# Kernel tuning notes

Measured on AMD Instinct MI355X. Metric: run time of the kernel, lower is better.

## Reference

```python
import jax, jax.numpy as jnp
import numpy as np

N = 100_000      # nodes
E = 1_600_000    # edges (before self-loops)
F_IN = 128       # num_features
H = 128          # nhid
G = 512          # graphs in batch
C = 10           # num_classes
EPS = 1e-5       # BatchNorm eps


def setup_inputs() -> dict:
    key = jax.random.key(0)
    ks = jax.random.split(key, 24)
    x = jax.random.normal(ks[0], (N, F_IN), jnp.float32)
    edge_index = jax.random.randint(ks[1], (2, E), 0, N, dtype=jnp.int64)
    batch = jnp.sort(jax.random.randint(ks[2], (N,), 0, G, dtype=jnp.int64))

    def lin(k, fi, fo):
        return jax.random.normal(k, (fi, fo), jnp.float32) / np.sqrt(fi).astype(np.float32)

    inp = dict(x=x, edge_index=edge_index, batch=batch)
    inp.update(
        W1=lin(ks[3], F_IN, H), b1=jnp.zeros((H,), jnp.float32),
        g1=jnp.ones((H,), jnp.float32), be1=jnp.zeros((H,), jnp.float32),
        W2=lin(ks[4], H, H), b2=jnp.zeros((H,), jnp.float32),
        g2=jnp.ones((H,), jnp.float32), be2=jnp.zeros((H,), jnp.float32),
        W3=lin(ks[5], H, H), b3=jnp.zeros((H,), jnp.float32),
        g3=jnp.ones((H,), jnp.float32), be3=jnp.zeros((H,), jnp.float32),
        gp=jnp.ones((H,), jnp.float32), bep=jnp.zeros((H,), jnp.float32),
        lw1=lin(ks[6], H, H), lb1=jnp.zeros((H,), jnp.float32),
        lw2=lin(ks[7], H, C), lb2=jnp.zeros((C,), jnp.float32),
    )
    return inp


def _batchnorm(h, g, b):
    # training-mode BatchNorm1d: batch stats, biased variance
    m = h.mean(axis=0)
    v = h.var(axis=0)
    return g * (h - m) * jax.lax.rsqrt(v + EPS) + b


def _gcn(h, W, b, src, dst, norm, n):
    # GCNConv: h @ W, then normalized gather-scatter aggregation
    h = h @ W
    msg = h[src] * norm[:, None]                     # [E+N, H] gather
    out = jax.ops.segment_sum(msg, dst, num_segments=n)
    return out + b


def reference(x, edge_index, batch, W1, b1, g1, be1, W2, b2, g2, be2,
              W3, b3, g3, be3, gp, bep, lw1, lb1, lw2, lb2):
    n = x.shape[0]
    loops = jnp.arange(n, dtype=edge_index.dtype)
    src = jnp.concatenate([edge_index[0], loops])
    dst = jnp.concatenate([edge_index[1], loops])
    # symmetric normalization D^{-1/2} (A+I) D^{-1/2}
    deg = jax.ops.segment_sum(jnp.ones_like(src, dtype=x.dtype), dst, num_segments=n)
    dis = jnp.where(deg > 0, jax.lax.rsqrt(jnp.maximum(deg, 1.0)), 0.0)
    norm = dis[src] * dis[dst]

    h = jax.nn.relu(_batchnorm(_gcn(x, W1, b1, src, dst, norm, n), g1, be1))
    h = jax.nn.relu(_batchnorm(_gcn(h, W2, b2, src, dst, norm, n), g2, be2))
    h = jax.nn.relu(_batchnorm(_gcn(h, W3, b3, src, dst, norm, n), g3, be3))

    # global_mean_pool over graph ids
    counts = jax.ops.segment_sum(jnp.ones((n,), x.dtype), batch, num_segments=G)
    pooled = jax.ops.segment_sum(h, batch, num_segments=G) / jnp.maximum(counts, 1.0)[:, None]

    z = _batchnorm(pooled, gp, bep)
    z = jax.nn.relu(z @ lw1 + lb1)
    # dropout_ratio=0.0 -> identity
    z = z @ lw2 + lb2
    return jax.nn.log_softmax(z, axis=-1)
```

## Files before the change

kernel.cpp:

```cpp
#include <hip/hip_runtime.h>
#include <hip/hip_bf16.h>
#include <cstdint>

#define HDIM 128

typedef __bf16 bf16x8 __attribute__((ext_vector_type(8)));
typedef unsigned short usx8 __attribute__((ext_vector_type(8)));
typedef float fx4 __attribute__((ext_vector_type(4)));

__device__ __forceinline__ float bf2f(unsigned short u) {
    unsigned int x = ((unsigned int)u) << 16;
    return __uint_as_float(x);
}
__device__ __forceinline__ unsigned short f2bf(float f) {
    unsigned int x = __float_as_uint(f);
    x += 0x7fffu + ((x >> 16) & 1u);
    return (unsigned short)(x >> 16);
}

__device__ __forceinline__ void detect_local(const unsigned int* xw, const unsigned int* eiw,
                                             int& f0, int& f1) {
    int sane = 0;
    for (int k = 0; k < 64; k++) {
        unsigned int w = xw[k];
        unsigned short ss[2] = {(unsigned short)(w & 0xffffu), (unsigned short)(w >> 16)};
        for (int q = 0; q < 2; q++) {
            int e = (ss[q] >> 7) & 0xFF;
            if ((ss[q] & 0x7fffu) == 0 || (e >= 100 && e <= 140)) sane++;
        }
    }
    f0 = (sane >= 110) ? 1 : 0;
    int zeros = 0;
    for (int k = 1; k < 64; k += 2)
        if (eiw[k] == 0) zeros++;
    f1 = (zeros >= 24) ? 1 : 0;
}

struct ParamTab {
    const void* p[15];
    int n[15];
    int off[15];
};

__global__ void phase1(const unsigned int* __restrict__ xw, const unsigned int* __restrict__ eiw,
                       const void* __restrict__ ei, const void* __restrict__ batch,
                       const void* __restrict__ W1, const void* __restrict__ W2,
                       const void* __restrict__ W3, ParamTab tab, int* __restrict__ flags,
                       float* __restrict__ gsumAll, int* __restrict__ Ct,
                       unsigned short* __restrict__ wconv, unsigned short* __restrict__ Wf,
                       int* __restrict__ goff, int* __restrict__ gcnt, int E, int N, int G,
                       int NB, int ntiles, int TILE) {
    __shared__ int h[1024];
    __shared__ int lf0s, lf1s;
    int b = blockIdx.x, t = threadIdx.x;
    if (t == 0) {
        int a0, a1;
        detect_local(xw, eiw, a0, a1);
        lf0s = a0;
        lf1s = a1;
    }
    __syncthreads();
    int lf0 = lf0s, lf1 = lf1s;
    if (b < ntiles) {
        for (int i = t; i < NB; i += 256) h[i] = 0;
        __syncthreads();
        int base = b * TILE;
        for (int i = t; i < TILE; i += 256) {
            int idx = base + i;
            if (idx < E) {
                int d = lf1 ? (int)((const long long*)ei)[(size_t)E + idx]
                            : ((const int*)ei)[(size_t)E + idx];
                atomicAdd(&h[d >> 9], 1);
            }
        }
        __syncthreads();
        for (int k = t; k < NB; k += 256) Ct[k * ntiles + b] = h[k];
    } else if (b < ntiles + 15) {
        int pb = b - ntiles;
        const void* src = tab.p[pb];
        int n = tab.n[pb];
        unsigned short* o = wconv + tab.off[pb];
        if (lf0) {
            const unsigned short* s = (const unsigned short*)src;
            for (int i = t; i < n; i += 256) o[i] = s[i];
        } else {
            const float* s = (const float*)src;
            for (int i = t; i < n; i += 256) o[i] = f2bf(s[i]);
        }
    } else if (b < ntiles + 17) {
        int gi = (b - ntiles - 15) * 256 + t;
        if (gi < G) {
            auto getb = [&](int i) -> int {
                return lf1 ? (int)((const long long*)batch)[i] : ((const int*)batch)[i];
            };
            auto lower = [&](int val) -> int {
                int lo = 0, hi = N;
                while (lo < hi) {
                    int mid = (lo + hi) >> 1;
                    if (getb(mid) < val) lo = mid + 1;
                    else hi = mid;
                }
                return lo;
            };
            int lo = lower(gi), hi = lower(gi + 1);
            goff[gi] = lo;
            gcnt[gi] = hi - lo;
        }
    } else if (b < ntiles + 17 + 24) {
        int idx = (b - ntiles - 17) * 256 + t;
        int layer = idx >> 11;
        int rem = idx & 2047;
        int kt = rem >> 9;
        int nt = (rem >> 6) & 7;
        int lane = rem & 63;
        const void* W = (layer == 0) ? W1 : ((layer == 1) ? W2 : W3);
        int row = lane & 15, quad = lane >> 4;
        unsigned short* o = Wf + ((size_t)layer * 2048 + (size_t)((kt * 8 + nt) * 64 + lane)) * 8;
#pragma unroll
        for (int j = 0; j < 8; j++) {
            int k = kt * 32 + quad * 8 + j;
            int off = k * HDIM + nt * 16 + row;
            o[j] = lf0 ? ((const unsigned short*)W)[off] : f2bf(((const float*)W)[off]);
        }
    } else {
        for (int i = t; i < 768; i += 256) gsumAll[i] = 0.f;
        if (t == 0) {
            flags[0] = lf0;
            flags[1] = lf1;
        }
    }
}

__global__ void scanA(const int* __restrict__ d, int* __restrict__ part, int L) {
    __shared__ int ls[256];
    int b = blockIdx.x, t = threadIdx.x;
    int base = b * 2048;
    int s = 0;
    for (int j = t; j < 2048; j += 256) {
        int i = base + j;
        if (i < L) s += d[i];
    }
    ls[t] = s;
    __syncthreads();
    for (int o = 128; o > 0; o >>= 1) {
        if (t < o) ls[t] += ls[t + o];
        __syncthreads();
    }
    if (t == 0) part[b] = ls[0];
}
__global__ void scan2(int* part, int nb) {
    __shared__ int ls[128];
    int t = threadIdx.x;
    int orig = (t < nb) ? part[t] : 0;
    ls[t] = orig;
    __syncthreads();
    for (int o = 1; o < 128; o <<= 1) {
        int v = (t >= o) ? ls[t - o] : 0;
        __syncthreads();
        ls[t] += v;
        __syncthreads();
    }
    if (t < nb) part[t] = ls[t] - orig;
}
__global__ void scanC(int* __restrict__ d, const int* __restrict__ part, int L) {
    __shared__ int ls[256];
    __shared__ int excl[256];
    int b = blockIdx.x, t = threadIdx.x;
    int i0 = b * 2048 + t * 8;
    int v[8];
    int s = 0;
#pragma unroll
    for (int q = 0; q < 8; q++) {
        v[q] = (i0 + q < L) ? d[i0 + q] : 0;
        s += v[q];
    }
    ls[t] = s;
    __syncthreads();
    if (t == 0) {
        int a = 0;
        for (int j = 0; j < 256; j++) { excl[j] = a; a += ls[j]; }
    }
    __syncthreads();
    int base = part[b] + excl[t];
#pragma unroll
    for (int q = 0; q < 8; q++) {
        if (i0 + q < L) d[i0 + q] = base;
        base += v[q];
    }
}

__global__ void p1_scatter(const void* __restrict__ ei, const int* __restrict__ flags,
                           const int* __restrict__ Ct, unsigned int* __restrict__ pairs, int E,
                           int NB, int ntiles, int TILE) {
    __shared__ int cur[1024];
    int tile = blockIdx.x, t = threadIdx.x;
    for (int i = t; i < NB; i += 256) cur[i] = Ct[i * ntiles + tile];
    __syncthreads();
    int base = tile * TILE;
    bool i64 = flags[1] != 0;
    for (int i = t; i < TILE; i += 256) {
        int idx = base + i;
        if (idx < E) {
            int s, d;
            if (i64) {
                s = (int)((const long long*)ei)[idx];
                d = (int)((const long long*)ei)[(size_t)E + idx];
            } else {
                s = ((const int*)ei)[idx];
                d = ((const int*)ei)[(size_t)E + idx];
            }
            int pos = atomicAdd(&cur[d >> 9], 1);
            pairs[pos] = ((unsigned)(d & 511) << 23) | (unsigned)s;
        }
    }
}

__global__ void p2_build(const unsigned int* __restrict__ pairs, const int* __restrict__ Ct,
                         int* __restrict__ csrc, int* __restrict__ offs, int* __restrict__ cnt,
                         float* __restrict__ dis, int E, int N, int NB, int ntiles) {
    __shared__ int hist[512];
    __shared__ int start[512];
    __shared__ int cur[512];
    __shared__ int ps[256];
    int b = blockIdx.x, t = threadIdx.x;
    int node0 = b * 512;
    for (int i = t; i < 512; i += 256) hist[i] = 0;
    __syncthreads();
    int lo = Ct[b * ntiles];
    int hi = (b + 1 < NB) ? Ct[(b + 1) * ntiles] : E;
    for (int i = lo + t; i < hi; i += 256) {
        atomicAdd(&hist[pairs[i] >> 23], 1);
    }
    __syncthreads();
    ps[t] = hist[2 * t] + hist[2 * t + 1];
    __syncthreads();
    for (int o = 1; o < 256; o <<= 1) {
        int v = (t >= o) ? ps[t - o] : 0;
        __syncthreads();
        ps[t] += v;
        __syncthreads();
    }
    int e = t ? ps[t - 1] : 0;
    start[2 * t] = e;
    start[2 * t + 1] = e + hist[2 * t];
    __syncthreads();
    for (int i = t; i < 512; i += 256) {
        cur[i] = 0;
        int node = node0 + i;
        if (node < N) {
            offs[node] = lo + start[i];
            cnt[node] = hist[i];
            dis[node] = rsqrtf((float)(hist[i] + 1));
        }
    }
    __syncthreads();
    for (int i = lo + t; i < hi; i += 256) {
        unsigned int p = pairs[i];
        int l = p >> 23;
        int pos = lo + start[l] + atomicAdd(&cur[l], 1);
        csrc[pos] = (int)(p & 0x7fffffu);
    }
}

__global__ __launch_bounds__(256) void mm_mfma(const void* __restrict__ A,
                                               const unsigned short* __restrict__ Wf,
                                               unsigned short* __restrict__ C, int M,
                                               const float* __restrict__ sc,
                                               const float* __restrict__ sh,
                                               const float* __restrict__ dis,
                                               const int* __restrict__ flags, int l0mode) {
    int gid = blockIdx.x * blockDim.x + threadIdx.x;
    int wave = gid >> 6;
    int lane = threadIdx.x & 63;
    int m0 = wave * 16;
    if (m0 >= M) return;
    int row = lane & 15, quad = lane >> 4;
    bool xfp32 = l0mode && !flags[0];
    const unsigned short* arow =
        (const unsigned short*)A + (size_t)(m0 + row) * HDIM + quad * 8;
    const float* arowf = (const float*)A + (size_t)(m0 + row) * HDIM + quad * 8;
    fx4 acc[8];
#pragma unroll
    for (int t = 0; t < 8; t++) acc[t] = (fx4){0.f, 0.f, 0.f, 0.f};
#pragma unroll
    for (int kt = 0; kt < 4; kt++) {
        bf16x8 a;
        if (xfp32) {
            fx4 f0 = *(const fx4*)(arowf + kt * 32);
            fx4 f1 = *(const fx4*)(arowf + kt * 32 + 4);
            usx8 t;
#pragma unroll
            for (int q = 0; q < 4; q++) t[q] = f2bf(f0[q]);
#pragma unroll
            for (int q = 0; q < 4; q++) t[4 + q] = f2bf(f1[q]);
            a = __builtin_bit_cast(bf16x8, t);
        } else {
            usx8 raw = *(const usx8*)(arow + kt * 32);
            if (!l0mode) {
                int col = kt * 32 + quad * 8;
                fx4 s0 = *(const fx4*)(sc + col);
                fx4 s1 = *(const fx4*)(sc + col + 4);
                fx4 h0 = *(const fx4*)(sh + col);
                fx4 h1 = *(const fx4*)(sh + col + 4);
                usx8 t;
#pragma unroll
                for (int q = 0; q < 4; q++)
                    t[q] = f2bf(fmaxf(s0[q] * bf2f(raw[q]) + h0[q], 0.f));
#pragma unroll
                for (int q = 0; q < 4; q++)
                    t[4 + q] = f2bf(fmaxf(s1[q] * bf2f(raw[4 + q]) + h1[q], 0.f));
                a = __builtin_bit_cast(bf16x8, t);
            } else {
                a = __builtin_bit_cast(bf16x8, raw);
            }
        }
        const unsigned short* wf = Wf + ((size_t)(kt * 8) * 64 + lane) * 8;
#pragma unroll
        for (int nt = 0; nt < 8; nt++) {
            bf16x8 b = __builtin_bit_cast(bf16x8, *(const usx8*)(wf + (size_t)nt * 64 * 8));
            acc[nt] = __builtin_amdgcn_mfma_f32_16x16x32_bf16(a, b, acc[nt], 0, 0, 0);
        }
    }
    float dsc[4];
#pragma unroll
    for (int r = 0; r < 4; r++) dsc[r] = dis[m0 + quad * 4 + r];
#pragma unroll
    for (int nt = 0; nt < 8; nt++) {
        int col = nt * 16 + row;
#pragma unroll
        for (int r = 0; r < 4; r++) {
            int m = m0 + quad * 4 + r;
            C[(size_t)m * HDIM + col] = f2bf(acc[nt][r] * dsc[r]);
        }
    }
}

__global__ __launch_bounds__(256) void aggregate(const unsigned short* __restrict__ hw,
                                                 const float* __restrict__ dis,
                                                 const int* __restrict__ offs,
                                                 const int* __restrict__ cnt,
                                                 const int* __restrict__ csrc,
                                                 const unsigned short* __restrict__ bias,
                                                 unsigned short* __restrict__ agg, int n) {
    int wv = (blockIdx.x * blockDim.x + threadIdx.x) >> 6;
    int lane = threadIdx.x & 63;
    int grp = lane >> 4, sub = lane & 15;
    int node = wv * 4 + grp;
    if (node >= n) return;
    int colb = sub * 8;
    usx8 sv = *(const usx8*)(hw + (size_t)node * HDIM + colb);
    float a[8];
#pragma unroll
    for (int q = 0; q < 8; q++) a[q] = bf2f(sv[q]);
    int o = offs[node], c = cnt[node];
    int s0 = (c > 0) ? csrc[o] : 0;
    int s1 = (c > 1) ? csrc[o + 1] : 0;
    int j = 0;
    while (j < c) {
        usx8 v0 = *(const usx8*)(hw + (size_t)s0 * HDIM + colb);
        usx8 v1 = *(const usx8*)(hw + (size_t)s1 * HDIM + colb);
        int s2 = (j + 2 < c) ? csrc[o + j + 2] : 0;
        int s3 = (j + 3 < c) ? csrc[o + j + 3] : 0;
#pragma unroll
        for (int q = 0; q < 8; q++) a[q] += bf2f(v0[q]);
        if (j + 1 < c) {
#pragma unroll
            for (int q = 0; q < 8; q++) a[q] += bf2f(v1[q]);
        }
        s0 = s2;
        s1 = s3;
        j += 2;
    }
    float di = dis[node];
    usx8 bv = *(const usx8*)(bias + colb);
    usx8 ov;
#pragma unroll
    for (int q = 0; q < 8; q++) ov[q] = f2bf(bf2f(bv[q]) + di * a[q]);
    *(usx8*)(agg + (size_t)node * HDIM + colb) = ov;
}

__global__ void col_stats(const unsigned short* __restrict__ agg, float* __restrict__ gsum,
                          float* __restrict__ gsq, int n) {
    int t = threadIdx.x;
    int c = t & 127, p = t >> 7;
    float s = 0.f, s2 = 0.f;
    int stride = gridDim.x * 2;
    for (int r = blockIdx.x * 2 + p; r < n; r += stride) {
        float v = bf2f(agg[(size_t)r * HDIM + c]);
        s += v;
        s2 += v * v;
    }
    __shared__ float ls[256], ls2[256];
    ls[t] = s;
    ls2[t] = s2;
    __syncthreads();
    if (t < 128) {
        atomicAdd(&gsum[t], ls[t] + ls[t + 128]);
        atomicAdd(&gsq[t], ls2[t] + ls2[t + 128]);
    }
}
__global__ void bn_finalize(const float* __restrict__ gsum, const float* __restrict__ gsq,
                            const unsigned short* __restrict__ g,
                            const unsigned short* __restrict__ be,
                            float* __restrict__ sc, float* __restrict__ sh, float invn) {
    int c = threadIdx.x;
    if (c < 128) {
        float m = gsum[c] * invn;
        float v = gsq[c] * invn - m * m;
        float s = bf2f(g[c]) * rsqrtf(v + 1e-5f);
        sc[c] = s;
        sh[c] = bf2f(be[c]) - m * s;
    }
}

__global__ void pool(const unsigned short* __restrict__ hin, const int* __restrict__ goff,
                     const int* __restrict__ gcnt, const float* __restrict__ sc,
                     const float* __restrict__ sh, float* __restrict__ pooled) {
    int g = blockIdx.x, t = threadIdx.x;
    int c = t & 127, p = t >> 7;
    float scale = sc[c], shift = sh[c];
    int s = goff[g], cn = gcnt[g];
    float acc = 0.f;
    for (int r = s + p; r < s + cn; r += 2)
        acc += fmaxf(scale * bf2f(hin[(size_t)r * HDIM + c]) + shift, 0.f);
    __shared__ float ls[256];
    ls[t] = acc;
    __syncthreads();
    if (t < 128) pooled[(size_t)g * HDIM + t] = (ls[t] + ls[t + 128]) / fmaxf((float)cn, 1.f);
}
__global__ void pooled_bn(const float* __restrict__ pooled, const unsigned short* __restrict__ g,
                          const unsigned short* __restrict__ be, float* __restrict__ psc,
                          float* __restrict__ psh, int G_) {
    int t = threadIdx.x;
    int c = t & 127, p = t >> 7;
    float s = 0.f, s2 = 0.f;
    for (int r = p; r < G_; r += 4) {
        float v = pooled[(size_t)r * HDIM + c];
        s += v;
        s2 += v * v;
    }
    __shared__ float ls[512], ls2[512];
    ls[t] = s;
    ls2[t] = s2;
    __syncthreads();
    if (t < 128) {
        float S = ls[t] + ls[t + 128] + ls[t + 256] + ls[t + 384];
        float S2 = ls2[t] + ls2[t + 128] + ls2[t + 256] + ls2[t + 384];
        float m = S / (float)G_;
        float v = S2 / (float)G_ - m * m;
        float sc = bf2f(g[t]) * rsqrtf(v + 1e-5f);
        psc[t] = sc;
        psh[t] = bf2f(be[t]) - m * sc;
    }
}
__global__ void mlp1(const float* __restrict__ pooled, const float* __restrict__ psc,
                     const float* __restrict__ psh, const unsigned short* __restrict__ lw1,
                     const unsigned short* __restrict__ lb1, float* __restrict__ z1) {
    int r = blockIdx.x, t = threadIdx.x;
    __shared__ float row[128];
    row[t] = psc[t] * pooled[(size_t)r * HDIM + t] + psh[t];
    __syncthreads();
    float acc = bf2f(lb1[t]);
    for (int k = 0; k < 128; k++) acc += row[k] * bf2f(lw1[k * HDIM + t]);
    z1[(size_t)r * HDIM + t] = fmaxf(acc, 0.f);
}
__global__ void mlp2(const float* __restrict__ z1, const unsigned short* __restrict__ lw2,
                     const unsigned short* __restrict__ lb2, void* __restrict__ out,
                     const int* __restrict__ flags) {
    int r = blockIdx.x, t = threadIdx.x;
    __shared__ float row[128];
    __shared__ float z2[10];
    __shared__ float lse;
    row[t] = z1[(size_t)r * HDIM + t];
    __syncthreads();
    if (t < 10) {
        float a = bf2f(lb2[t]);
        for (int k = 0; k < 128; k++) a += row[k] * bf2f(lw2[k * 10 + t]);
        z2[t] = a;
    }
    __syncthreads();
    if (t == 0) {
        float m = z2[0];
        for (int j = 1; j < 10; j++) m = fmaxf(m, z2[j]);
        float s = 0.f;
        for (int j = 0; j < 10; j++) s += expf(z2[j] - m);
        lse = m + logf(s);
    }
    __syncthreads();
    if (t < 10) {
        float v = z2[t] - lse;
        if (flags[0]) ((unsigned short*)out)[r * 10 + t] = f2bf(v);
        else ((float*)out)[r * 10 + t] = v;
    }
}

extern "C" void kernel_launch(void* const* d_in, const int* in_sizes, int n_in,
                              void* d_out, int out_size, void* d_ws, size_t ws_size,
                              hipStream_t stream) {
    const void* x = d_in[0];
    const void* ei = d_in[1];
    const void* batch = d_in[2];

    int N_ = in_sizes[2];
    int E_ = in_sizes[1] / 2;
    int G_ = out_size / 10;

    const int TILE = 4096;
    int NB = (N_ + 511) / 512;
    int ntiles = (E_ + TILE - 1) / TILE;
    int L = NB * ntiles;
    int nscan = (L + 2047) / 2048;

    char* ws = (char*)d_ws;
    auto alloc = [&](size_t bytes) -> char* {
        char* p = ws;
        ws += (bytes + 255) & ~(size_t)255;
        return p;
    };
    int* flags = (int*)alloc(256);
    float* dis = (float*)alloc((size_t)N_ * 4);
    int* offs = (int*)alloc((size_t)N_ * 4);
    int* cnt = (int*)alloc((size_t)N_ * 4);
    int* part = (int*)alloc(4096);
    int* Ct = (int*)alloc((size_t)L * 4);
    unsigned int* pairs = (unsigned int*)alloc((size_t)E_ * 4);
    int* csrc = (int*)alloc((size_t)E_ * 4);
    unsigned short* hw = (unsigned short*)alloc((size_t)N_ * HDIM * 2);
    unsigned short* aggbuf = (unsigned short*)alloc((size_t)N_ * HDIM * 2);
    unsigned short* wconv = (unsigned short*)alloc(70000 * 2);
    unsigned short* wfrag = (unsigned short*)alloc(3 * HDIM * HDIM * 2);
    float* gsumAll = (float*)alloc(768 * 4);
    float* bsc = (float*)alloc(128 * 4);
    float* bsh = (float*)alloc(128 * 4);
    int* gcnt = (int*)alloc((size_t)G_ * 4);
    int* goff = (int*)alloc((size_t)G_ * 4);
    float* pooled = (float*)alloc((size_t)G_ * HDIM * 4);
    float* psc = (float*)alloc(128 * 4);
    float* psh = (float*)alloc(128 * 4);
    float* z1 = (float*)alloc((size_t)G_ * HDIM * 4);

    const int oB = 49152;
    const int oLB1 = oB + 1408;
    const int oLW1 = oLB1 + 128;
    const int oLW2 = oLW1 + 16384;
    const int oLB2 = oLW2 + 1280;

    ParamTab tab;
    const int srcIdx[15] = {4, 5, 6, 8, 9, 10, 12, 13, 14, 15, 16, 18, 17, 19, 20};
    const int dstOff[15] = {oB + 0, oB + 128, oB + 256,
                            oB + 384, oB + 512, oB + 640,
                            oB + 768, oB + 896, oB + 1024,
                            oB + 1152, oB + 1280,
                            oLB1, oLW1, oLW2, oLB2};
    for (int i = 0; i < 15; i++) {
        tab.p[i] = d_in[srcIdx[i]];
        tab.n[i] = in_sizes[srcIdx[i]];
        tab.off[i] = dstOff[i];
    }

    int gb = (G_ + 255) / 256;
    int p1_grid = ntiles + 15 + 2 + 24 + 1;
    phase1<<<p1_grid, 256, 0, stream>>>((const unsigned int*)x, (const unsigned int*)ei, ei,
                                        batch, d_in[3], d_in[7], d_in[11], tab, flags, gsumAll,
                                        Ct, wconv, wfrag, goff, gcnt, E_, N_, G_, NB, ntiles,
                                        TILE);
    (void)gb;

    scanA<<<nscan, 256, 0, stream>>>(Ct, part, L);
    scan2<<<1, 128, 0, stream>>>(part, nscan);
    scanC<<<nscan, 256, 0, stream>>>(Ct, part, L);
    p1_scatter<<<ntiles, 256, 0, stream>>>(ei, flags, Ct, pairs, E_, NB, ntiles, TILE);
    p2_build<<<NB, 256, 0, stream>>>(pairs, Ct, csrc, offs, cnt, dis, E_, N_, NB, ntiles);

    int mm_blocks = (((N_ + 15) / 16) * 64 + 255) / 256;
    int agg_blocks = (N_ + 15) / 16;
    float invn = 1.f / (float)N_;

    for (int l = 0; l < 3; l++) {
        const void* A = (l == 0) ? x : (const void*)aggbuf;
        mm_mfma<<<mm_blocks, 256, 0, stream>>>(A, wfrag + (size_t)l * HDIM * HDIM, hw, N_,
                                               bsc, bsh, dis, flags, (l == 0) ? 1 : 0);
        aggregate<<<agg_blocks, 256, 0, stream>>>(hw, dis, offs, cnt, csrc,
                                                  wconv + oB + l * 384, aggbuf, N_);
        float* gsum = gsumAll + l * 256;
        col_stats<<<512, 256, 0, stream>>>(aggbuf, gsum, gsum + 128, N_);
        bn_finalize<<<1, 128, 0, stream>>>(gsum, gsum + 128, wconv + oB + l * 384 + 128,
                                           wconv + oB + l * 384 + 256, bsc, bsh, invn);
    }

    pool<<<G_, 256, 0, stream>>>(aggbuf, goff, gcnt, bsc, bsh, pooled);
    pooled_bn<<<1, 512, 0, stream>>>(pooled, wconv + oB + 1152, wconv + oB + 1280, psc, psh, G_);
    mlp1<<<G_, 128, 0, stream>>>(pooled, psc, psh, wconv + oLW1, wconv + oLB1, z1);
    mlp2<<<G_, 128, 0, stream>>>(z1, wconv + oLW2, wconv + oLB2, d_out, flags);
}
```

Measured before the change: 612.8 us.

## Fuse BN stats into aggregation, BN finalize into matmul, and simplify CSR scan

Column statistics for BatchNorm are now accumulated inside the aggregation kernel, a grid-stride loop with 768 blocks that spreads its atomics across 8 replicas. This removes the separate col_stats pass over the 100k×128 activation. BN finalize moves into the prologue of the next matmul and of the pool kernel, the two MLP kernels are merged into one, and the three-kernel scan becomes a per-bucket scan with block totals re-scanned inside consumers. The matmul also stages its output through LDS so that global stores are coalesced 16-byte writes. In exchange, every block redundantly recomputes the small scale/shift and prefix-sum values, and the aggregation gather is unrolled to four edges per step.

```diff
diff --git a/kernel.cpp b/kernel.cpp
--- a/kernel.cpp
+++ b/kernel.cpp
@@ -123,7 +123,7 @@
             o[j] = lf0 ? ((const unsigned short*)W)[off] : f2bf(((const float*)W)[off]);
         }
     } else {
-        for (int i = t; i < 768; i += 256) gsumAll[i] = 0.f;
+        for (int i = t; i < 6144; i += 256) gsumAll[i] = 0.f;
         if (t == 0) {
             flags[0] = lf0;
             flags[1] = lf1;
@@ -131,70 +131,39 @@
     }
 }
 
-__global__ void scanA(const int* __restrict__ d, int* __restrict__ part, int L) {
-    __shared__ int ls[256];
+__global__ void s1_scan(int* __restrict__ Ct, int* __restrict__ btot, int NB, int ntiles) {
+    __shared__ int buf[512];
     int b = blockIdx.x, t = threadIdx.x;
-    int base = b * 2048;
-    int s = 0;
-    for (int j = t; j < 2048; j += 256) {
-        int i = base + j;
-        if (i < L) s += d[i];
-    }
-    ls[t] = s;
-    __syncthreads();
-    for (int o = 128; o > 0; o >>= 1) {
-        if (t < o) ls[t] += ls[t + o];
-        __syncthreads();
-    }
-    if (t == 0) part[b] = ls[0];
-}
-__global__ void scan2(int* part, int nb) {
-    __shared__ int ls[128];
-    int t = threadIdx.x;
-    int orig = (t < nb) ? part[t] : 0;
-    ls[t] = orig;
-    __syncthreads();
-    for (int o = 1; o < 128; o <<= 1) {
-        int v = (t >= o) ? ls[t - o] : 0;
-        __syncthreads();
-        ls[t] += v;
-        __syncthreads();
-    }
-    if (t < nb) part[t] = ls[t] - orig;
-}
-__global__ void scanC(int* __restrict__ d, const int* __restrict__ part, int L) {
-    __shared__ int ls[256];
-    __shared__ int excl[256];
-    int b = blockIdx.x, t = threadIdx.x;
-    int i0 = b * 2048 + t * 8;
-    int v[8];
-    int s = 0;
-#pragma unroll
-    for (int q = 0; q < 8; q++) {
-        v[q] = (i0 + q < L) ? d[i0 + q] : 0;
-        s += v[q];
-    }
-    ls[t] = s;
-    __syncthreads();
-    if (t == 0) {
-        int a = 0;
-        for (int j = 0; j < 256; j++) { excl[j] = a; a += ls[j]; }
-    }
-    __syncthreads();
-    int base = part[b] + excl[t];
-#pragma unroll
-    for (int q = 0; q < 8; q++) {
-        if (i0 + q < L) d[i0 + q] = base;
-        base += v[q];
-    }
+    int v = (t < ntiles) ? Ct[b * ntiles + t] : 0;
+    buf[t] = v;
+    __syncthreads();
+    for (int o = 1; o < 512; o <<= 1) {
+        int a = (t >= o) ? buf[t - o] : 0;
+        __syncthreads();
+        buf[t] += a;
+        __syncthreads();
+    }
+    if (t < ntiles) Ct[b * ntiles + t] = buf[t] - v;
+    if (t == 0) btot[b] = buf[511];
 }
 
 __global__ void p1_scatter(const void* __restrict__ ei, const int* __restrict__ flags,
-                           const int* __restrict__ Ct, unsigned int* __restrict__ pairs, int E,
-                           int NB, int ntiles, int TILE) {
+                           const int* __restrict__ Ct, const int* __restrict__ btot,
+                           unsigned int* __restrict__ pairs, int E, int NB, int ntiles,
+                           int TILE) {
     __shared__ int cur[1024];
+    __shared__ int bb[256];
     int tile = blockIdx.x, t = threadIdx.x;
-    for (int i = t; i < NB; i += 256) cur[i] = Ct[i * ntiles + tile];
+    int v = (t < NB) ? btot[t] : 0;
+    bb[t] = v;
+    __syncthreads();
+    for (int o = 1; o < 256; o <<= 1) {
+        int a = (t >= o) ? bb[t - o] : 0;
+        __syncthreads();
+        bb[t] += a;
+        __syncthreads();
+    }
+    if (t < NB) cur[t] = (bb[t] - v) + Ct[t * ntiles + tile];
     __syncthreads();
     int base = tile * TILE;
     bool i64 = flags[1] != 0;
@@ -215,19 +184,31 @@
     }
 }
 
-__global__ void p2_build(const unsigned int* __restrict__ pairs, const int* __restrict__ Ct,
+__global__ void p2_build(const unsigned int* __restrict__ pairs, const int* __restrict__ btot,
                          int* __restrict__ csrc, int* __restrict__ offs, int* __restrict__ cnt,
-                         float* __restrict__ dis, int E, int N, int NB, int ntiles) {
+                         float* __restrict__ dis, int E, int N, int NB) {
     __shared__ int hist[512];
     __shared__ int start[512];
     __shared__ int cur[512];
     __shared__ int ps[256];
+    __shared__ int bb[256];
+    __shared__ int sh_excl[256];
     int b = blockIdx.x, t = threadIdx.x;
     int node0 = b * 512;
+    int v = (t < NB) ? btot[t] : 0;
+    bb[t] = v;
+    __syncthreads();
+    for (int o = 1; o < 256; o <<= 1) {
+        int a = (t >= o) ? bb[t - o] : 0;
+        __syncthreads();
+        bb[t] += a;
+        __syncthreads();
+    }
+    sh_excl[t] = bb[t] - v;
     for (int i = t; i < 512; i += 256) hist[i] = 0;
     __syncthreads();
-    int lo = Ct[b * ntiles];
-    int hi = (b + 1 < NB) ? Ct[(b + 1) * ntiles] : E;
+    int lo = sh_excl[b];
+    int hi = lo + ((b < NB) ? btot[b] : 0);
     for (int i = lo + t; i < hi; i += 256) {
         atomicAdd(&hist[pairs[i] >> 23], 1);
     }
@@ -235,9 +216,9 @@
     ps[t] = hist[2 * t] + hist[2 * t + 1];
     __syncthreads();
     for (int o = 1; o < 256; o <<= 1) {
-        int v = (t >= o) ? ps[t - o] : 0;
-        __syncthreads();
-        ps[t] += v;
+        int a = (t >= o) ? ps[t - o] : 0;
+        __syncthreads();
+        ps[t] += a;
         __syncthreads();
     }
     int e = t ? ps[t - 1] : 0;
@@ -265,51 +246,70 @@
 __global__ __launch_bounds__(256) void mm_mfma(const void* __restrict__ A,
                                                const unsigned short* __restrict__ Wf,
                                                unsigned short* __restrict__ C, int M,
-                                               const float* __restrict__ sc,
-                                               const float* __restrict__ sh,
+                                               const float* __restrict__ gsumPrev,
+                                               const unsigned short* __restrict__ gamma,
+                                               const unsigned short* __restrict__ beta,
                                                const float* __restrict__ dis,
-                                               const int* __restrict__ flags, int l0mode) {
-    int gid = blockIdx.x * blockDim.x + threadIdx.x;
+                                               const int* __restrict__ flags, int l0mode,
+                                               float invn) {
+    __shared__ float scs[128], shs[128];
+    __shared__ unsigned short ldsC[4 * 16 * 136];
+    int t = threadIdx.x;
+    if (!l0mode && t < 128) {
+        float s = 0.f, s2 = 0.f;
+#pragma unroll
+        for (int r = 0; r < 8; r++) {
+            s += gsumPrev[r * 256 + t];
+            s2 += gsumPrev[r * 256 + 128 + t];
+        }
+        float m = s * invn;
+        float vv = s2 * invn - m * m;
+        float sc = bf2f(gamma[t]) * rsqrtf(vv + 1e-5f);
+        scs[t] = sc;
+        shs[t] = bf2f(beta[t]) - m * sc;
+    }
+    __syncthreads();
+    int gid = blockIdx.x * blockDim.x + t;
     int wave = gid >> 6;
-    int lane = threadIdx.x & 63;
+    int lane = t & 63;
+    int wv = t >> 6;
     int m0 = wave * 16;
     if (m0 >= M) return;
     int row = lane & 15, quad = lane >> 4;
     bool xfp32 = l0mode && !flags[0];
-    const unsigned short* arow =
-        (const unsigned short*)A + (size_t)(m0 + row) * HDIM + quad * 8;
+    const unsigned short* arow = (const unsigned short*)A + (size_t)(m0 + row) * HDIM + quad * 8;
     const float* arowf = (const float*)A + (size_t)(m0 + row) * HDIM + quad * 8;
     fx4 acc[8];
 #pragma unroll
-    for (int t = 0; t < 8; t++) acc[t] = (fx4){0.f, 0.f, 0.f, 0.f};
+    for (int k = 0; k < 8; k++) acc[k] = (fx4){0.f, 0.f, 0.f, 0.f};
 #pragma unroll
     for (int kt = 0; kt < 4; kt++) {
         bf16x8 a;
         if (xfp32) {
             fx4 f0 = *(const fx4*)(arowf + kt * 32);
             fx4 f1 = *(const fx4*)(arowf + kt * 32 + 4);
-            usx8 t;
-#pragma unroll
-            for (int q = 0; q < 4; q++) t[q] = f2bf(f0[q]);
-#pragma unroll
-            for (int q = 0; q < 4; q++) t[4 + q] = f2bf(f1[q]);
-            a = __builtin_bit_cast(bf16x8, t);
+            usx8 tt;
+#pragma unroll
+            for (int q = 0; q < 4; q++) tt[q] = f2bf(f0[q]);
+#pragma unroll
+            for (int q = 0; q < 4; q++) tt[4 + q] = f2bf(f1[q]);
+            a = __builtin_bit_cast(bf16x8, tt);
         } else {
             usx8 raw = *(const usx8*)(arow + kt * 32);
             if (!l0mode) {
                 int col = kt * 32 + quad * 8;
-                fx4 s0 = *(const fx4*)(sc + col);
-                fx4 s1 = *(const fx4*)(sc + col + 4);
-                fx4 h0 = *(const fx4*)(sh + col);
-                fx4 h1 = *(const fx4*)(sh + col + 4);
-                usx8 t;
+                fx4 s0 = *(const fx4*)&scs[col];
+                fx4 s1 = *(const fx4*)&scs[col + 4];
+                fx4 h0 = *(const fx4*)&shs[col];
+                fx4 h1 = *(const fx4*)&shs[col + 4];
+                usx8 tt;
 #pragma unroll
                 for (int q = 0; q < 4; q++)
-                    t[q] = f2bf(fmaxf(s0[q] * bf2f(raw[q]) + h0[q], 0.f));
+                    tt[q] = f2bf(fmaxf(s0[q] * bf2f(raw[q]) + h0[q], 0.f));
 #pragma unroll
                 for (int q = 0; q < 4; q++)
-                    t[4 + q] = f2bf(fmaxf(s1[q] * bf2f(raw[4 + q]) + h1[q], 0.f));
-                a = __builtin_bit_cast(bf16x8, t);
+                    tt[4 + q] = f2bf(fmaxf(s1[q] * bf2f(raw[4 + q]) + h1[q], 0.f));
+                a = __builtin_bit_cast(bf16x8, tt);
             } else {
                 a = __builtin_bit_cast(bf16x8, raw);
             }
@@ -317,21 +317,29 @@
         const unsigned short* wf = Wf + ((size_t)(kt * 8) * 64 + lane) * 8;
 #pragma unroll
         for (int nt = 0; nt < 8; nt++) {
-            bf16x8 b = __builtin_bit_cast(bf16x8, *(const usx8*)(wf + (size_t)nt * 64 * 8));
-            acc[nt] = __builtin_amdgcn_mfma_f32_16x16x32_bf16(a, b, acc[nt], 0, 0, 0);
+            bf16x8 bfr = __builtin_bit_cast(bf16x8, *(const usx8*)(wf + (size_t)nt * 64 * 8));
+            acc[nt] = __builtin_amdgcn_mfma_f32_16x16x32_bf16(a, bfr, acc[nt], 0, 0, 0);
         }
     }
     float dsc[4];
 #pragma unroll
     for (int r = 0; r < 4; r++) dsc[r] = dis[m0 + quad * 4 + r];
+    unsigned short* lw = ldsC + wv * 16 * 136;
 #pragma unroll
     for (int nt = 0; nt < 8; nt++) {
         int col = nt * 16 + row;
 #pragma unroll
         for (int r = 0; r < 4; r++) {
-            int m = m0 + quad * 4 + r;
-            C[(size_t)m * HDIM + col] = f2bf(acc[nt][r] * dsc[r]);
-        }
+            lw[(quad * 4 + r) * 136 + col] = f2bf(acc[nt][r] * dsc[r]);
+        }
+    }
+    int row16 = lane >> 2;
+    int seg = lane & 3;
+    const unsigned short* src = lw + row16 * 136 + seg * 32;
+    unsigned short* dst = C + (size_t)(m0 + row16) * HDIM + seg * 32;
+#pragma unroll
+    for (int k = 0; k < 4; k++) {
+        *(usx8*)(dst + k * 8) = *(const usx8*)(src + k * 8);
     }
 }
 
@@ -341,89 +349,121 @@
                                                  const int* __restrict__ cnt,
                                                  const int* __restrict__ csrc,
                                                  const unsigned short* __restrict__ bias,
-                                                 unsigned short* __restrict__ agg, int n) {
-    int wv = (blockIdx.x * blockDim.x + threadIdx.x) >> 6;
-    int lane = threadIdx.x & 63;
+                                                 unsigned short* __restrict__ agg,
+                                                 float* __restrict__ gsum8, int n) {
+    __shared__ float red[16 * 128];
+    int t = threadIdx.x;
+    int lane = t & 63;
+    int wv = t >> 6;
     int grp = lane >> 4, sub = lane & 15;
-    int node = wv * 4 + grp;
-    if (node >= n) return;
     int colb = sub * 8;
-    usx8 sv = *(const usx8*)(hw + (size_t)node * HDIM + colb);
-    float a[8];
-#pragma unroll
-    for (int q = 0; q < 8; q++) a[q] = bf2f(sv[q]);
-    int o = offs[node], c = cnt[node];
-    int s0 = (c > 0) ? csrc[o] : 0;
-    int s1 = (c > 1) ? csrc[o + 1] : 0;
-    int j = 0;
-    while (j < c) {
-        usx8 v0 = *(const usx8*)(hw + (size_t)s0 * HDIM + colb);
-        usx8 v1 = *(const usx8*)(hw + (size_t)s1 * HDIM + colb);
-        int s2 = (j + 2 < c) ? csrc[o + j + 2] : 0;
-        int s3 = (j + 3 < c) ? csrc[o + j + 3] : 0;
-#pragma unroll
-        for (int q = 0; q < 8; q++) a[q] += bf2f(v0[q]);
-        if (j + 1 < c) {
-#pragma unroll
-            for (int q = 0; q < 8; q++) a[q] += bf2f(v1[q]);
-        }
-        s0 = s2;
-        s1 = s3;
-        j += 2;
-    }
-    float di = dis[node];
     usx8 bv = *(const usx8*)(bias + colb);
-    usx8 ov;
-#pragma unroll
-    for (int q = 0; q < 8; q++) ov[q] = f2bf(bf2f(bv[q]) + di * a[q]);
-    *(usx8*)(agg + (size_t)node * HDIM + colb) = ov;
-}
-
-__global__ void col_stats(const unsigned short* __restrict__ agg, float* __restrict__ gsum,
-                          float* __restrict__ gsq, int n) {
-    int t = threadIdx.x;
+    float csum[8], csq[8];
+#pragma unroll
+    for (int q = 0; q < 8; q++) {
+        csum[q] = 0.f;
+        csq[q] = 0.f;
+    }
+    int stride = gridDim.x * 16;
+    for (int node = blockIdx.x * 16 + wv * 4 + grp; node < n; node += stride) {
+        usx8 sv = *(const usx8*)(hw + (size_t)node * HDIM + colb);
+        float a[8];
+#pragma unroll
+        for (int q = 0; q < 8; q++) a[q] = bf2f(sv[q]);
+        int o = offs[node], c = cnt[node];
+        int s0 = (c > 0) ? csrc[o] : 0;
+        int s1 = (c > 1) ? csrc[o + 1] : 0;
+        int s2 = (c > 2) ? csrc[o + 2] : 0;
+        int s3 = (c > 3) ? csrc[o + 3] : 0;
+        int j = 0;
+        while (j < c) {
+            usx8 v0 = *(const usx8*)(hw + (size_t)s0 * HDIM + colb);
+            usx8 v1 = *(const usx8*)(hw + (size_t)s1 * HDIM + colb);
+            usx8 v2 = *(const usx8*)(hw + (size_t)s2 * HDIM + colb);
+            usx8 v3 = *(const usx8*)(hw + (size_t)s3 * HDIM + colb);
+            s0 = (j + 4 < c) ? csrc[o + j + 4] : 0;
+            s1 = (j + 5 < c) ? csrc[o + j + 5] : 0;
+            s2 = (j + 6 < c) ? csrc[o + j + 6] : 0;
+            s3 = (j + 7 < c) ? csrc[o + j + 7] : 0;
+#pragma unroll
+            for (int q = 0; q < 8; q++) a[q] += bf2f(v0[q]);
+            if (j + 1 < c) {
+#pragma unroll
+                for (int q = 0; q < 8; q++) a[q] += bf2f(v1[q]);
+            }
+            if (j + 2 < c) {
+#pragma unroll
+                for (int q = 0; q < 8; q++) a[q] += bf2f(v2[q]);
+            }
+            if (j + 3 < c) {
+#pragma unroll
+                for (int q = 0; q < 8; q++) a[q] += bf2f(v3[q]);
+            }
+            j += 4;
+        }
+        float di = dis[node];
+        usx8 ov;
+#pragma unroll
+        for (int q = 0; q < 8; q++) {
+            float val = bf2f(bv[q]) + di * a[q];
+            ov[q] = f2bf(val);
+            float vr = bf2f(ov[q]);
+            csum[q] += vr;
+            csq[q] += vr * vr;
+        }
+        *(usx8*)(agg + (size_t)node * HDIM + colb) = ov;
+    }
+    int gidx = wv * 4 + grp;
+    int rep = (blockIdx.x & 7) * 256;
+#pragma unroll
+    for (int q = 0; q < 8; q++) red[gidx * 128 + colb + q] = csum[q];
+    __syncthreads();
+    if (t < 128) {
+        float s = 0.f;
+#pragma unroll
+        for (int g = 0; g < 16; g++) s += red[g * 128 + t];
+        atomicAdd(&gsum8[rep + t], s);
+    }
+    __syncthreads();
+#pragma unroll
+    for (int q = 0; q < 8; q++) red[gidx * 128 + colb + q] = csq[q];
+    __syncthreads();
+    if (t < 128) {
+        float s = 0.f;
+#pragma unroll
+        for (int g = 0; g < 16; g++) s += red[g * 128 + t];
+        atomicAdd(&gsum8[rep + 128 + t], s);
+    }
+}
+
+__global__ void pool(const unsigned short* __restrict__ hin, const int* __restrict__ goff,
+                     const int* __restrict__ gcnt, const float* __restrict__ gsum3,
+                     const unsigned short* __restrict__ gamma,
+                     const unsigned short* __restrict__ beta, float* __restrict__ pooled,
+                     float invn) {
+    __shared__ float scs[128], shs[128];
+    __shared__ float ls[256];
+    int g = blockIdx.x, t = threadIdx.x;
+    if (t < 128) {
+        float s = 0.f, s2 = 0.f;
+#pragma unroll
+        for (int r = 0; r < 8; r++) {
+            s += gsum3[r * 256 + t];
+            s2 += gsum3[r * 256 + 128 + t];
+        }
+        float m = s * invn;
+        float vv = s2 * invn - m * m;
+        float sc = bf2f(gamma[t]) * rsqrtf(vv + 1e-5f);
+        scs[t] = sc;
+        shs[t] = bf2f(beta[t]) - m * sc;
+    }
+    __syncthreads();
     int c = t & 127, p = t >> 7;
-    float s = 0.f, s2 = 0.f;
-    int stride = gridDim.x * 2;
-    for (int r = blockIdx.x * 2 + p; r < n; r += stride) {
-        float v = bf2f(agg[(size_t)r * HDIM + c]);
-        s += v;
-        s2 += v * v;
-    }
-    __shared__ float ls[256], ls2[256];
-    ls[t] = s;
-    ls2[t] = s2;
-    __syncthreads();
-    if (t < 128) {
-        atomicAdd(&gsum[t], ls[t] + ls[t + 128]);
-        atomicAdd(&gsq[t], ls2[t] + ls2[t + 128]);
-    }
-}
-__global__ void bn_finalize(const float* __restrict__ gsum, const float* __restrict__ gsq,
-                            const unsigned short* __restrict__ g,
-                            const unsigned short* __restrict__ be,
-                            float* __restrict__ sc, float* __restrict__ sh, float invn) {
-    int c = threadIdx.x;
-    if (c < 128) {
-        float m = gsum[c] * invn;
-        float v = gsq[c] * invn - m * m;
-        float s = bf2f(g[c]) * rsqrtf(v + 1e-5f);
-        sc[c] = s;
-        sh[c] = bf2f(be[c]) - m * s;
-    }
-}
-
-__global__ void pool(const unsigned short* __restrict__ hin, const int* __restrict__ goff,
-                     const int* __restrict__ gcnt, const float* __restrict__ sc,
-                     const float* __restrict__ sh, float* __restrict__ pooled) {
-    int g = blockIdx.x, t = threadIdx.x;
-    int c = t & 127, p = t >> 7;
-    float scale = sc[c], shift = sh[c];
+    float scale = scs[c], shift = shs[c];
     int s = goff[g], cn = gcnt[g];
     float acc = 0.f;
     for (int r = s + p; r < s + cn; r += 2)
         acc += fmaxf(scale * bf2f(hin[(size_t)r * HDIM + c]) + shift, 0.f);
-    __shared__ float ls[256];
     ls[t] = acc;
     __syncthreads();
     if (t < 128) pooled[(size_t)g * HDIM + t] = (ls[t] + ls[t + 128]) / fmaxf((float)cn, 1.f);
@@ -453,29 +493,26 @@
         psh[t] = bf2f(be[t]) - m * sc;
     }
 }
-__global__ void mlp1(const float* __restrict__ pooled, const float* __restrict__ psc,
-                     const float* __restrict__ psh, const unsigned short* __restrict__ lw1,
-                     const unsigned short* __restrict__ lb1, float* __restrict__ z1) {
+__global__ void mlp12(const float* __restrict__ pooled, const float* __restrict__ psc,
+                      const float* __restrict__ psh, const unsigned short* __restrict__ lw1,
+                      const unsigned short* __restrict__ lb1,
+                      const unsigned short* __restrict__ lw2,
+                      const unsigned short* __restrict__ lb2, void* __restrict__ out,
+                      const int* __restrict__ flags) {
     int r = blockIdx.x, t = threadIdx.x;
     __shared__ float row[128];
+    __shared__ float z1s[128];
+    __shared__ float z2[10];
+    __shared__ float lse;
     row[t] = psc[t] * pooled[(size_t)r * HDIM + t] + psh[t];
     __syncthreads();
     float acc = bf2f(lb1[t]);
     for (int k = 0; k < 128; k++) acc += row[k] * bf2f(lw1[k * HDIM + t]);
-    z1[(size_t)r * HDIM + t] = fmaxf(acc, 0.f);
-}
-__global__ void mlp2(const float* __restrict__ z1, const unsigned short* __restrict__ lw2,
-                     const unsigned short* __restrict__ lb2, void* __restrict__ out,
-                     const int* __restrict__ flags) {
-    int r = blockIdx.x, t = threadIdx.x;
-    __shared__ float row[128];
-    __shared__ float z2[10];
-    __shared__ float lse;
-    row[t] = z1[(size_t)r * HDIM + t];
+    z1s[t] = fmaxf(acc, 0.f);
     __syncthreads();
     if (t < 10) {
         float a = bf2f(lb2[t]);
-        for (int k = 0; k < 128; k++) a += row[k] * bf2f(lw2[k * 10 + t]);
+        for (int k = 0; k < 128; k++) a += z1s[k] * bf2f(lw2[k * 10 + t]);
         z2[t] = a;
     }
     __syncthreads();
@@ -509,7 +546,6 @@
     int NB = (N_ + 511) / 512;
     int ntiles = (E_ + TILE - 1) / TILE;
     int L = NB * ntiles;
-    int nscan = (L + 2047) / 2048;
 
     char* ws = (char*)d_ws;
     auto alloc = [&](size_t bytes) -> char* {
@@ -521,23 +557,20 @@
     float* dis = (float*)alloc((size_t)N_ * 4);
     int* offs = (int*)alloc((size_t)N_ * 4);
     int* cnt = (int*)alloc((size_t)N_ * 4);
-    int* part = (int*)alloc(4096);
     int* Ct = (int*)alloc((size_t)L * 4);
+    int* btot = (int*)alloc(1024);
     unsigned int* pairs = (unsigned int*)alloc((size_t)E_ * 4);
     int* csrc = (int*)alloc((size_t)E_ * 4);
     unsigned short* hw = (unsigned short*)alloc((size_t)N_ * HDIM * 2);
     unsigned short* aggbuf = (unsigned short*)alloc((size_t)N_ * HDIM * 2);
     unsigned short* wconv = (unsigned short*)alloc(70000 * 2);
     unsigned short* wfrag = (unsigned short*)alloc(3 * HDIM * HDIM * 2);
-    float* gsumAll = (float*)alloc(768 * 4);
-    float* bsc = (float*)alloc(128 * 4);
-    float* bsh = (float*)alloc(128 * 4);
+    float* gsumAll = (float*)alloc(6144 * 4);
     int* gcnt = (int*)alloc((size_t)G_ * 4);
     int* goff = (int*)alloc((size_t)G_ * 4);
     float* pooled = (float*)alloc((size_t)G_ * HDIM * 4);
     float* psc = (float*)alloc(128 * 4);
     float* psh = (float*)alloc(128 * 4);
-    float* z1 = (float*)alloc((size_t)G_ * HDIM * 4);
 
     const int oB = 49152;
     const int oLB1 = oB + 1408;
@@ -558,38 +591,33 @@
         tab.off[i] = dstOff[i];
     }
 
-    int gb = (G_ + 255) / 256;
     int p1_grid = ntiles + 15 + 2 + 24 + 1;
     phase1<<<p1_grid, 256, 0, stream>>>((const unsigned int*)x, (const unsigned int*)ei, ei,
                                         batch, d_in[3], d_in[7], d_in[11], tab, flags, gsumAll,
                                         Ct, wconv, wfrag, goff, gcnt, E_, N_, G_, NB, ntiles,
                                         TILE);
-    (void)gb;
-
-    scanA<<<nscan, 256, 0, stream>>>(Ct, part, L);
-    scan2<<<1, 128, 0, stream>>>(part, nscan);
-    scanC<<<nscan, 256, 0, stream>>>(Ct, part, L);
-    p1_scatter<<<ntiles, 256, 0, stream>>>(ei, flags, Ct, pairs, E_, NB, ntiles, TILE);
-    p2_build<<<NB, 256, 0, stream>>>(pairs, Ct, csrc, offs, cnt, dis, E_, N_, NB, ntiles);
+    s1_scan<<<NB, 512, 0, stream>>>(Ct, btot, NB, ntiles);
+    p1_scatter<<<ntiles, 256, 0, stream>>>(ei, flags, Ct, btot, pairs, E_, NB, ntiles, TILE);
+    p2_build<<<NB, 256, 0, stream>>>(pairs, btot, csrc, offs, cnt, dis, E_, N_, NB);
 
     int mm_blocks = (((N_ + 15) / 16) * 64 + 255) / 256;
-    int agg_blocks = (N_ + 15) / 16;
     float invn = 1.f / (float)N_;
 
     for (int l = 0; l < 3; l++) {
         const void* A = (l == 0) ? x : (const void*)aggbuf;
-        mm_mfma<<<mm_blocks, 256, 0, stream>>>(A, wfrag + (size_t)l * HDIM * HDIM, hw, N_,
-                                               bsc, bsh, dis, flags, (l == 0) ? 1 : 0);
-        aggregate<<<agg_blocks, 256, 0, stream>>>(hw, dis, offs, cnt, csrc,
-                                                  wconv + oB + l * 384, aggbuf, N_);
-        float* gsum = gsumAll + l * 256;
-        col_stats<<<512, 256, 0, stream>>>(aggbuf, gsum, gsum + 128, N_);
-        bn_finalize<<<1, 128, 0, stream>>>(gsum, gsum + 128, wconv + oB + l * 384 + 128,
-                                           wconv + oB + l * 384 + 256, bsc, bsh, invn);
-    }
-
-    pool<<<G_, 256, 0, stream>>>(aggbuf, goff, gcnt, bsc, bsh, pooled);
+        const float* gp = (l == 0) ? nullptr : (gsumAll + (size_t)(l - 1) * 2048);
+        const unsigned short* gam = wconv + oB + (l ? (l - 1) * 384 + 128 : 0);
+        const unsigned short* bet = wconv + oB + (l ? (l - 1) * 384 + 256 : 0);
+        mm_mfma<<<mm_blocks, 256, 0, stream>>>(A, wfrag + (size_t)l * HDIM * HDIM, hw, N_, gp,
+                                               gam, bet, dis, flags, (l == 0) ? 1 : 0, invn);
+        aggregate<<<768, 256, 0, stream>>>(hw, dis, offs, cnt, csrc, wconv + oB + l * 384,
+                                           aggbuf, gsumAll + (size_t)l * 2048, N_);
+    }
+
+    pool<<<G_, 256, 0, stream>>>(aggbuf, goff, gcnt, gsumAll + 2 * 2048,
+                                 wconv + oB + 2 * 384 + 128, wconv + oB + 2 * 384 + 256, pooled,
+                                 invn);
     pooled_bn<<<1, 512, 0, stream>>>(pooled, wconv + oB + 1152, wconv + oB + 1280, psc, psh, G_);
-    mlp1<<<G_, 128, 0, stream>>>(pooled, psc, psh, wconv + oLW1, wconv + oLB1, z1);
-    mlp2<<<G_, 128, 0, stream>>>(z1, wconv + oLW2, wconv + oLB2, d_out, flags);
-}
+    mlp12<<<G_, 128, 0, stream>>>(pooled, psc, psh, wconv + oLW1, wconv + oLB1, wconv + oLW2,
+                                  wconv + oLB2, d_out, flags);
+}
```

Result: faster. 514.5 us (-16.0%).
